# Kernel tuning notes

Hardware: AMD Instinct MI355X
Metric: run time of the kernel (lower is better)

Reference implementation:

```python
import jax, jax.numpy as jnp
import numpy as np

# Semantics of GPTQ Marlin 2:4 int4 GEMM: W_dense[K,N] has exactly 2 nonzeros per
# group of 4 along K. Compressed int4 values (q-8)*scale are stored packed 8-per-int32
# in B [K/16, N]; meta [K/4, N] in [0,6) selects which pair of the 4 positions is
# nonzero (index into the 6 combinations). s [K/groupsize, N] are group scales.

_PAIRS = jnp.array([[0, 1], [0, 2], [0, 3], [1, 2], [1, 3], [2, 3]], dtype=jnp.int32)


def _dequant_24(B, meta, s):
    Kd16, N = B.shape
    K = Kd16 * 16
    # unpack 8 nibbles per int32 -> [K/2, N] compressed values
    shifts = (jnp.arange(8, dtype=jnp.int32) * 4)[None, :, None]
    nib = (B[:, None, :] >> shifts) & 0xF            # [K/16, 8, N]
    vals = nib.reshape(K // 2, N).astype(jnp.float32) - 8.0  # symmetric zero-point 8
    gs = K // s.shape[0]                              # original groupsize
    scale = jnp.repeat(s, gs // 2, axis=0)            # [K/2, N] (compressed K dim)
    deq = (vals * scale).reshape(K // 4, 2, N)        # 2 values per group of 4
    pos = _PAIRS[meta]                                # [K/4, N, 2] positions in [0,4)
    oh = jax.nn.one_hot(pos, 4, dtype=jnp.float32)    # [K/4, N, 2, 4]
    W = jnp.einsum('gjn,gnjp->gpn', deq, oh)          # scatter into group slots
    return W.reshape(K, N)


def setup_inputs() -> dict:
    key = jax.random.key(0)
    k0, k1, k2, k3, k4 = jax.random.split(key, 5)
    M, K, N, GS = 8192, 4096, 4096, 128
    A = jax.random.normal(k0, (M, K), dtype=jnp.float32)
    B = jax.random.randint(k1, (K // 16, N), 0, 2147483647, dtype=jnp.int32)
    meta = jax.random.randint(k2, (K // 4, N), 0, 6, dtype=jnp.int32)
    s = jax.random.uniform(k3, (K // GS, N), dtype=jnp.float32, minval=0.005, maxval=0.02)
    bias = jax.random.normal(k4, (N,), dtype=jnp.float32)
    return {"A": A, "B": B, "meta": meta, "s": s, "bias": bias}


def reference(A, B, meta, s, bias):
    W = _dequant_24(B, meta, s)          # [K, N] dense 2:4-sparse dequantized weight
    return jnp.matmul(A, W, preferred_element_type=jnp.float32) + bias
```

## Files before the change

kernel.cpp:

```cpp
#include <hip/hip_runtime.h>

typedef _Float16 h16;
typedef __attribute__((ext_vector_type(8))) _Float16 h16x8;
typedef __attribute__((ext_vector_type(4))) float f32x4;
typedef unsigned int u32;

#define BARRIER() __builtin_amdgcn_s_barrier()
#define SCHEDB()  __builtin_amdgcn_sched_barrier(0)

__global__ __launch_bounds__(256) void cvtA_kernel(const float* __restrict__ A,
                                                   h16* __restrict__ Ah, int total8) {
  int stride = gridDim.x * blockDim.x;
  for (int i = blockIdx.x * blockDim.x + threadIdx.x; i < total8; i += stride) {
    const f32x4* p = (const f32x4*)(A + (size_t)i * 8);
    f32x4 v0 = p[0], v1 = p[1];
    h16x8 o;
    o[0] = (h16)v0[0]; o[1] = (h16)v0[1]; o[2] = (h16)v0[2]; o[3] = (h16)v0[3];
    o[4] = (h16)v1[0]; o[5] = (h16)v1[1]; o[6] = (h16)v1[2]; o[7] = (h16)v1[3];
    *(h16x8*)(Ah + (size_t)i * 8) = o;
  }
}

__global__ __launch_bounds__(256) void dequant_kernel(const int* __restrict__ Bq,
    const int* __restrict__ meta, const float* __restrict__ s,
    h16* __restrict__ Wt, int K, int N, int chunksPerGroup) {
  int n = blockIdx.x * 256 + threadIdx.x;
  int chunk = blockIdx.y;
  u32 w0 = (u32)Bq[(size_t)(chunk * 2) * N + n];
  u32 w1 = (u32)Bq[(size_t)(chunk * 2 + 1) * N + n];
  float sc = s[(size_t)(chunk / chunksPerGroup) * N + n];
  h16 out[32];
#pragma unroll
  for (int gi = 0; gi < 8; ++gi) {
    int g = chunk * 8 + gi;
    int mm = meta[(size_t)g * N + n];
    u32 w = (gi < 4) ? w0 : w1;
    int j0 = (2 * gi) & 7;
    float d0 = (float)((int)((w >> (4 * j0)) & 0xFu) - 8) * sc;
    float d1 = (float)((int)((w >> (4 * j0 + 4)) & 0xFu) - 8) * sc;
    u32 enc = (0xED9C84u >> (4 * mm)) & 0xFu;
    int p0 = (int)(enc & 3u), p1 = (int)(enc >> 2);
#pragma unroll
    for (int p = 0; p < 4; ++p) {
      float v = (p == p0) ? d0 : ((p == p1) ? d1 : 0.0f);
      out[gi * 4 + p] = (h16)v;
    }
  }
  h16* dst = Wt + (size_t)n * K + chunk * 32;
  *(h16x8*)(dst + 0)  = *(h16x8*)(out + 0);
  *(h16x8*)(dst + 8)  = *(h16x8*)(out + 8);
  *(h16x8*)(dst + 16) = *(h16x8*)(out + 16);
  *(h16x8*)(dst + 24) = *(h16x8*)(out + 24);
}

__global__ __launch_bounds__(512, 2) void gemm_kernel(const h16* __restrict__ A,
    const h16* __restrict__ Wt, const float* __restrict__ bias,
    float* __restrict__ C, int M, int N, int K) {
  __shared__ alignas(16) h16 As[4][256 * 32];
  __shared__ alignas(16) h16 Bs[4][256 * 32];

  const int nTilesN = N >> 8;
  const int nwg = gridDim.x;
  int bid = blockIdx.x;
  int wg = (bid & 7) * (nwg >> 3) + (bid >> 3);
  int tm = wg / nTilesN, tn = wg - tm * nTilesN;

  const int tid = threadIdx.x;
  const int lane = tid & 63, w = tid >> 6;
  const int wr = w >> 2, wc = w & 3;

  const int srow = tid >> 2;
  const int ssw = ((tid & 3) << 4) ^ (((tid >> 3) & 3) << 4);
  const char* gA = (const char*)(A + ((size_t)(tm * 256) + srow) * K) + ssw;
  const char* gB = (const char*)(Wt + ((size_t)(tn * 256) + srow) * K) + ssw;
  const size_t j1off = (size_t)128 * K * 2;
  const int ldsoff = tid * 16;

#define STAGE_A(t_) do { int sl_ = (t_) & 3;                                   \
    const char* src_ = gA + (size_t)(t_) * 64;                                 \
    char* dst_ = (char*)&As[sl_][0] + ldsoff;                                  \
    __builtin_amdgcn_global_load_lds(                                          \
        (const __attribute__((address_space(1))) void*)src_,                   \
        (__attribute__((address_space(3))) void*)dst_, 16, 0, 0);              \
    __builtin_amdgcn_global_load_lds(                                          \
        (const __attribute__((address_space(1))) void*)(src_ + j1off),         \
        (__attribute__((address_space(3))) void*)(dst_ + 8192), 16, 0, 0);     \
  } while (0)
#define STAGE_B(t_) do { int sl_ = (t_) & 3;                                   \
    const char* src_ = gB + (size_t)(t_) * 64;                                 \
    char* dst_ = (char*)&Bs[sl_][0] + ldsoff;                                  \
    __builtin_amdgcn_global_load_lds(                                          \
        (const __attribute__((address_space(1))) void*)src_,                   \
        (__attribute__((address_space(3))) void*)dst_, 16, 0, 0);              \
    __builtin_amdgcn_global_load_lds(                                          \
        (const __attribute__((address_space(1))) void*)(src_ + j1off),         \
        (__attribute__((address_space(3))) void*)(dst_ + 8192), 16, 0, 0);     \
  } while (0)

  const int cbR = ((lane >> 4) << 4) ^ (((lane >> 1) & 3) << 4);
  const int arow = wr * 128 + (lane & 15);
  const int brow = wc * 64 + (lane & 15);

  f32x4 acc[8][4] = {};

  const int NT = K >> 5;
  STAGE_A(0); STAGE_B(0);
  STAGE_A(1); STAGE_B(1);
  STAGE_A(2); STAGE_B(2);
  asm volatile("s_waitcnt vmcnt(8)" ::: "memory");
  SCHEDB();
  BARRIER();
  SCHEDB();

  for (int t = 0; t < NT; ++t) {
    const int slot = t & 3;
    const char* a_s = (const char*)&As[slot][0];
    const char* b_s = (const char*)&Bs[slot][0];
    h16x8 af[4], bf[4];

#pragma unroll
    for (int m = 0; m < 4; ++m)
      af[m] = *(const h16x8*)(a_s + (size_t)(arow + m * 16) * 64 + cbR);
#pragma unroll
    for (int n = 0; n < 4; ++n)
      bf[n] = *(const h16x8*)(b_s + (size_t)(brow + n * 16) * 64 + cbR);
    if (t + 3 < NT) STAGE_A(t + 3);
    SCHEDB();
    BARRIER();
    asm volatile("s_waitcnt lgkmcnt(0)" ::: "memory");
    SCHEDB();
    __builtin_amdgcn_s_setprio(1);
#pragma unroll
    for (int m = 0; m < 4; ++m)
#pragma unroll
      for (int n = 0; n < 4; ++n)
        acc[m][n] = __builtin_amdgcn_mfma_f32_16x16x32_f16(af[m], bf[n], acc[m][n], 0, 0, 0);
    __builtin_amdgcn_s_setprio(0);
    SCHEDB();
    BARRIER();
    SCHEDB();

#pragma unroll
    for (int m = 0; m < 4; ++m)
      af[m] = *(const h16x8*)(a_s + (size_t)(arow + 64 + m * 16) * 64 + cbR);
    if (t + 3 < NT) STAGE_B(t + 3);
    SCHEDB();
    BARRIER();
    asm volatile("s_waitcnt lgkmcnt(0)" ::: "memory");
    SCHEDB();
    __builtin_amdgcn_s_setprio(1);
#pragma unroll
    for (int m = 0; m < 4; ++m)
#pragma unroll
      for (int n = 0; n < 4; ++n)
        acc[4 + m][n] = __builtin_amdgcn_mfma_f32_16x16x32_f16(af[m], bf[n], acc[4 + m][n], 0, 0, 0);
    __builtin_amdgcn_s_setprio(0);
    SCHEDB();
    if (t + 3 < NT) {
      asm volatile("s_waitcnt vmcnt(8)" ::: "memory");
    } else if (t + 2 < NT) {
      asm volatile("s_waitcnt vmcnt(4)" ::: "memory");
    } else if (t + 1 < NT) {
      asm volatile("s_waitcnt vmcnt(0)" ::: "memory");
    }
    SCHEDB();
    BARRIER();
    SCHEDB();
  }

  int colBase = tn * 256 + wc * 64 + (lane & 15);
  int rowBase = tm * 256 + wr * 128 + (lane >> 4) * 4;
#pragma unroll
  for (int n = 0; n < 4; ++n) {
    float bv = bias[colBase + n * 16];
#pragma unroll
    for (int m = 0; m < 8; ++m) {
#pragma unroll
      for (int j = 0; j < 4; ++j) {
        C[(size_t)(rowBase + m * 16 + j) * N + colBase + n * 16] = acc[m][n][j] + bv;
      }
    }
  }
#undef STAGE_A
#undef STAGE_B
}

extern "C" void kernel_launch(void* const* d_in, const int* in_sizes, int n_in,
                              void* d_out, int out_size, void* d_ws, size_t ws_size,
                              hipStream_t stream) {
  const float* A = (const float*)d_in[0];
  const int* Bq = (const int*)d_in[1];
  const int* meta = (const int*)d_in[2];
  const float* s = (const float*)d_in[3];
  const float* bias = (const float*)d_in[4];
  float* C = (float*)d_out;

  const int N = in_sizes[4];
  const int K = (int)(((long long)in_sizes[1] * 16) / N);
  const int M = (int)((long long)in_sizes[0] / K);
  const int sRows = (int)((long long)in_sizes[3] / N);
  const int chunksPerGroup = (K / sRows) / 32;

  h16* Ah = (h16*)d_ws;
  h16* Wt = Ah + (size_t)M * K;

  cvtA_kernel<<<2048, 256, 0, stream>>>(A, Ah, (M * K) / 8);

  dim3 dgrid(N / 256, K / 32);
  dequant_kernel<<<dgrid, 256, 0, stream>>>(Bq, meta, s, Wt, K, N, chunksPerGroup);

  int grid = (M / 256) * (N / 256);
  gemm_kernel<<<grid, 512, 0, stream>>>(Ah, Wt, bias, C, M, N, K);
}
```

Before: 317.9 us.

## Restructure GEMM mainloop to BK=64 double-buffered half-tiles with four-phase MFMA schedule

New measurement: 295.0 us. 7.2% less time.

```diff
diff --git a/kernel.cpp b/kernel.cpp
--- a/kernel.cpp
+++ b/kernel.cpp
@@ -56,8 +56,8 @@
 __global__ __launch_bounds__(512, 2) void gemm_kernel(const h16* __restrict__ A,
     const h16* __restrict__ Wt, const float* __restrict__ bias,
     float* __restrict__ C, int M, int N, int K) {
-  __shared__ alignas(16) h16 As[4][256 * 32];
-  __shared__ alignas(16) h16 Bs[4][256 * 32];
+  __shared__ alignas(16) h16 As[2 * 2 * 8192];
+  __shared__ alignas(16) h16 Bs[2 * 2 * 8192];
 
   const int nTilesN = N >> 8;
   const int nwg = gridDim.x;
@@ -69,62 +69,64 @@
   const int lane = tid & 63, w = tid >> 6;
   const int wr = w >> 2, wc = w & 3;
 
-  const int srow = tid >> 2;
-  const int ssw = ((tid & 3) << 4) ^ (((tid >> 3) & 3) << 4);
-  const char* gA = (const char*)(A + ((size_t)(tm * 256) + srow) * K) + ssw;
-  const char* gB = (const char*)(Wt + ((size_t)(tn * 256) + srow) * K) + ssw;
-  const size_t j1off = (size_t)128 * K * 2;
-  const int ldsoff = tid * 16;
-
-#define STAGE_A(t_) do { int sl_ = (t_) & 3;                                   \
-    const char* src_ = gA + (size_t)(t_) * 64;                                 \
-    char* dst_ = (char*)&As[sl_][0] + ldsoff;                                  \
-    __builtin_amdgcn_global_load_lds(                                          \
-        (const __attribute__((address_space(1))) void*)src_,                   \
-        (__attribute__((address_space(3))) void*)dst_, 16, 0, 0);              \
-    __builtin_amdgcn_global_load_lds(                                          \
-        (const __attribute__((address_space(1))) void*)(src_ + j1off),         \
-        (__attribute__((address_space(3))) void*)(dst_ + 8192), 16, 0, 0);     \
-  } while (0)
-#define STAGE_B(t_) do { int sl_ = (t_) & 3;                                   \
-    const char* src_ = gB + (size_t)(t_) * 64;                                 \
-    char* dst_ = (char*)&Bs[sl_][0] + ldsoff;                                  \
-    __builtin_amdgcn_global_load_lds(                                          \
-        (const __attribute__((address_space(1))) void*)src_,                   \
-        (__attribute__((address_space(3))) void*)dst_, 16, 0, 0);              \
-    __builtin_amdgcn_global_load_lds(                                          \
-        (const __attribute__((address_space(1))) void*)(src_ + j1off),         \
-        (__attribute__((address_space(3))) void*)(dst_ + 8192), 16, 0, 0);     \
-  } while (0)
-
-  const int cbR = ((lane >> 4) << 4) ^ (((lane >> 1) & 3) << 4);
-  const int arow = wr * 128 + (lane & 15);
-  const int brow = wc * 64 + (lane & 15);
+  const int i0 = tid >> 3;
+  const int sigma = (tid & 7) ^ ((tid >> 3) & 7);
+  const h16* gA_t = A + ((size_t)(tm * 256) + i0) * K + sigma * 8;
+  const int rB0 = ((i0 >> 5) << 6) + (i0 & 31);
+  const h16* gB_t = Wt + ((size_t)(tn * 256) + rB0) * K + sigma * 8;
+  const int tid8 = tid * 8;
+  const size_t rowK128 = (size_t)128 * K;
+
+#define GLOAD(SRC, DST) __builtin_amdgcn_global_load_lds(                      \
+    (const __attribute__((address_space(1))) void*)(SRC),                      \
+    (__attribute__((address_space(3))) void*)(DST), 16, 0, 0)
+
+#define STAGE_A(T_, mh_) do {                                                  \
+    const h16* s_ = gA_t + (size_t)((mh_) * 64) * K + (T_) * 64;               \
+    h16* d_ = As + ((((T_) & 1) * 2 + (mh_)) * 8192) + tid8;                   \
+    GLOAD(s_, d_); GLOAD(s_ + rowK128, d_ + 4096); } while (0)
+
+#define STAGE_B(T_, nh_) do {                                                  \
+    const h16* s_ = gB_t + (size_t)((nh_) * 32) * K + (T_) * 64;               \
+    h16* d_ = Bs + ((((T_) & 1) * 2 + (nh_)) * 8192) + tid8;                   \
+    GLOAD(s_, d_); GLOAD(s_ + rowK128, d_ + 4096); } while (0)
+
+  const int ln15 = lane & 15, l16 = lane >> 4, l7 = lane & 7;
+  const int aRow = (wr * 64 + ln15) * 64;
+  const int bRow = (wc * 32 + ln15) * 64;
+  const int sl0 = ((0 + l16) ^ l7) * 8;
+  const int sl1 = ((4 + l16) ^ l7) * 8;
 
   f32x4 acc[8][4] = {};
-
-  const int NT = K >> 5;
-  STAGE_A(0); STAGE_B(0);
-  STAGE_A(1); STAGE_B(1);
-  STAGE_A(2); STAGE_B(2);
-  asm volatile("s_waitcnt vmcnt(8)" ::: "memory");
+  const int NT = K >> 6;
+
+  STAGE_A(0, 0); STAGE_B(0, 0); STAGE_B(0, 1); STAGE_A(0, 1);
+  STAGE_A(1, 0); STAGE_B(1, 0); STAGE_B(1, 1);
+  asm volatile("s_waitcnt vmcnt(6)" ::: "memory");
   SCHEDB();
   BARRIER();
   SCHEDB();
 
-  for (int t = 0; t < NT; ++t) {
-    const int slot = t & 3;
-    const char* a_s = (const char*)&As[slot][0];
-    const char* b_s = (const char*)&Bs[slot][0];
-    h16x8 af[4], bf[4];
-
-#pragma unroll
-    for (int m = 0; m < 4; ++m)
-      af[m] = *(const h16x8*)(a_s + (size_t)(arow + m * 16) * 64 + cbR);
-#pragma unroll
-    for (int n = 0; n < 4; ++n)
-      bf[n] = *(const h16x8*)(b_s + (size_t)(brow + n * 16) * 64 + cbR);
-    if (t + 3 < NT) STAGE_A(t + 3);
+  for (int T = 0; T < NT; ++T) {
+    const int buf = T & 1;
+    const h16* a0 = As + (buf * 2 + 0) * 8192;
+    const h16* a1 = As + (buf * 2 + 1) * 8192;
+    const h16* b0 = Bs + (buf * 2 + 0) * 8192;
+    const h16* b1 = Bs + (buf * 2 + 1) * 8192;
+    h16x8 af[4][2], bf0[2][2], bf1[2][2];
+
+#pragma unroll
+    for (int m = 0; m < 4; ++m) {
+      af[m][0] = *(const h16x8*)(a0 + aRow + m * 1024 + sl0);
+      af[m][1] = *(const h16x8*)(a0 + aRow + m * 1024 + sl1);
+    }
+#pragma unroll
+    for (int n = 0; n < 2; ++n) {
+      bf0[n][0] = *(const h16x8*)(b0 + bRow + n * 1024 + sl0);
+      bf0[n][1] = *(const h16x8*)(b0 + bRow + n * 1024 + sl1);
+    }
+    if (T + 1 < NT) STAGE_A(T + 1, 1);
+    asm volatile("s_waitcnt lgkmcnt(8)" ::: "memory");
     SCHEDB();
     BARRIER();
     asm volatile("s_waitcnt lgkmcnt(0)" ::: "memory");
@@ -133,17 +135,20 @@
 #pragma unroll
     for (int m = 0; m < 4; ++m)
 #pragma unroll
-      for (int n = 0; n < 4; ++n)
-        acc[m][n] = __builtin_amdgcn_mfma_f32_16x16x32_f16(af[m], bf[n], acc[m][n], 0, 0, 0);
-    __builtin_amdgcn_s_setprio(0);
-    SCHEDB();
-    BARRIER();
-    SCHEDB();
-
-#pragma unroll
-    for (int m = 0; m < 4; ++m)
-      af[m] = *(const h16x8*)(a_s + (size_t)(arow + 64 + m * 16) * 64 + cbR);
-    if (t + 3 < NT) STAGE_B(t + 3);
+      for (int n = 0; n < 2; ++n) {
+        acc[m][n] = __builtin_amdgcn_mfma_f32_16x16x32_f16(af[m][0], bf0[n][0], acc[m][n], 0, 0, 0);
+        acc[m][n] = __builtin_amdgcn_mfma_f32_16x16x32_f16(af[m][1], bf0[n][1], acc[m][n], 0, 0, 0);
+      }
+    __builtin_amdgcn_s_setprio(0);
+    SCHEDB();
+    BARRIER();
+
+#pragma unroll
+    for (int n = 0; n < 2; ++n) {
+      bf1[n][0] = *(const h16x8*)(b1 + bRow + n * 1024 + sl0);
+      bf1[n][1] = *(const h16x8*)(b1 + bRow + n * 1024 + sl1);
+    }
+    if (T + 2 < NT) STAGE_A(T + 2, 0);
     SCHEDB();
     BARRIER();
     asm volatile("s_waitcnt lgkmcnt(0)" ::: "memory");
@@ -152,15 +157,53 @@
 #pragma unroll
     for (int m = 0; m < 4; ++m)
 #pragma unroll
-      for (int n = 0; n < 4; ++n)
-        acc[4 + m][n] = __builtin_amdgcn_mfma_f32_16x16x32_f16(af[m], bf[n], acc[4 + m][n], 0, 0, 0);
-    __builtin_amdgcn_s_setprio(0);
-    SCHEDB();
-    if (t + 3 < NT) {
-      asm volatile("s_waitcnt vmcnt(8)" ::: "memory");
-    } else if (t + 2 < NT) {
-      asm volatile("s_waitcnt vmcnt(4)" ::: "memory");
-    } else if (t + 1 < NT) {
+      for (int n = 0; n < 2; ++n) {
+        acc[m][2 + n] = __builtin_amdgcn_mfma_f32_16x16x32_f16(af[m][0], bf1[n][0], acc[m][2 + n], 0, 0, 0);
+        acc[m][2 + n] = __builtin_amdgcn_mfma_f32_16x16x32_f16(af[m][1], bf1[n][1], acc[m][2 + n], 0, 0, 0);
+      }
+    __builtin_amdgcn_s_setprio(0);
+    SCHEDB();
+    BARRIER();
+
+#pragma unroll
+    for (int m = 0; m < 4; ++m) {
+      af[m][0] = *(const h16x8*)(a1 + aRow + m * 1024 + sl0);
+      af[m][1] = *(const h16x8*)(a1 + aRow + m * 1024 + sl1);
+    }
+    if (T + 2 < NT) STAGE_B(T + 2, 0);
+    SCHEDB();
+    BARRIER();
+    asm volatile("s_waitcnt lgkmcnt(0)" ::: "memory");
+    SCHEDB();
+    __builtin_amdgcn_s_setprio(1);
+#pragma unroll
+    for (int m = 0; m < 4; ++m)
+#pragma unroll
+      for (int n = 0; n < 2; ++n) {
+        acc[4 + m][2 + n] = __builtin_amdgcn_mfma_f32_16x16x32_f16(af[m][0], bf1[n][0], acc[4 + m][2 + n], 0, 0, 0);
+        acc[4 + m][2 + n] = __builtin_amdgcn_mfma_f32_16x16x32_f16(af[m][1], bf1[n][1], acc[4 + m][2 + n], 0, 0, 0);
+      }
+    __builtin_amdgcn_s_setprio(0);
+    SCHEDB();
+    BARRIER();
+
+    if (T + 2 < NT) STAGE_B(T + 2, 1);
+    SCHEDB();
+    BARRIER();
+    SCHEDB();
+    __builtin_amdgcn_s_setprio(1);
+#pragma unroll
+    for (int m = 0; m < 4; ++m)
+#pragma unroll
+      for (int n = 0; n < 2; ++n) {
+        acc[4 + m][n] = __builtin_amdgcn_mfma_f32_16x16x32_f16(af[m][0], bf0[n][0], acc[4 + m][n], 0, 0, 0);
+        acc[4 + m][n] = __builtin_amdgcn_mfma_f32_16x16x32_f16(af[m][1], bf0[n][1], acc[4 + m][n], 0, 0, 0);
+      }
+    __builtin_amdgcn_s_setprio(0);
+    SCHEDB();
+    if (T < NT - 2) {
+      asm volatile("s_waitcnt vmcnt(6)" ::: "memory");
+    } else if (T == NT - 2) {
       asm volatile("s_waitcnt vmcnt(0)" ::: "memory");
     }
     SCHEDB();
@@ -168,8 +211,8 @@
     SCHEDB();
   }
 
-  int colBase = tn * 256 + wc * 64 + (lane & 15);
-  int rowBase = tm * 256 + wr * 128 + (lane >> 4) * 4;
+  int colBase = tn * 256 + wc * 64 + ln15;
+  int rowBase = tm * 256 + wr * 128 + l16 * 4;
 #pragma unroll
   for (int n = 0; n < 4; ++n) {
     float bv = bias[colBase + n * 16];
@@ -183,6 +226,7 @@
   }
 #undef STAGE_A
 #undef STAGE_B
+#undef GLOAD
 }
 
 extern "C" void kernel_launch(void* const* d_in, const int* in_sizes, int n_in,
```
